# Kernel tuning notes

Measured on AMD Instinct MI355X. Metric: run time of the kernel, lower is better.

## Reference

```python
import jax, jax.numpy as jnp
import numpy as np

N_STATE = 2048
N_HEAD = 16
HEAD_DIM = N_STATE // N_HEAD  # 128
ROPE_THETA = 10000.0


def setup_inputs() -> dict:
    key = jax.random.key(0)
    ks = jax.random.split(key, 8)
    B, S, D = 2, 2048, N_STATE
    scale = 1.0 / np.sqrt(D)
    x = jax.random.normal(ks[0], (B, S, D), dtype=jnp.float32)
    Wq = jax.random.normal(ks[1], (D, D), dtype=jnp.float32) * scale
    bq = jnp.zeros((D,), dtype=jnp.float32)
    Wk = jax.random.normal(ks[2], (D, D), dtype=jnp.float32) * scale  # key has no bias
    Wv = jax.random.normal(ks[3], (D, D), dtype=jnp.float32) * scale
    bv = jnp.zeros((D,), dtype=jnp.float32)
    Wo = jax.random.normal(ks[4], (D, D), dtype=jnp.float32) * scale
    bo = jnp.zeros((D,), dtype=jnp.float32)
    return {"x": x, "Wq": Wq, "bq": bq, "Wk": Wk, "Wv": Wv, "bv": bv, "Wo": Wo, "bo": bo}


def _rope(t, pos):
    # t: [B, S, H, hd]; torchtune-style interleaved rotary (pairs of adjacent dims)
    hd = t.shape[-1]
    inv_freq = 1.0 / (ROPE_THETA ** (jnp.arange(0, hd, 2, dtype=jnp.float32) / hd))  # [hd/2]
    ang = pos[:, None] * inv_freq[None, :]                    # [S, hd/2]
    cos = jnp.cos(ang)[None, :, None, :].astype(t.dtype)       # [1,S,1,hd/2]
    sin = jnp.sin(ang)[None, :, None, :].astype(t.dtype)
    t1 = t[..., 0::2]
    t2 = t[..., 1::2]
    rot = jnp.stack([t1 * cos - t2 * sin, t2 * cos + t1 * sin], axis=-1)
    return rot.reshape(t.shape)


def reference(x, Wq, bq, Wk, Wv, bv, Wo, bo):
    B, S, D = x.shape
    H, hd = N_HEAD, D // N_HEAD
    q = (x @ Wq.T + bq).reshape(B, S, H, hd)
    k = (x @ Wk.T).reshape(B, S, H, hd)
    v = (x @ Wv.T + bv).reshape(B, S, H, hd)
    pos = jnp.arange(S, dtype=jnp.float32)
    q = _rope(q, pos)
    k = _rope(k, pos)
    # [B,H,S,hd]
    q = q.transpose(0, 2, 1, 3)
    k = k.transpose(0, 2, 1, 3)
    v = v.transpose(0, 2, 1, 3)
    scale = 1.0 / jnp.sqrt(jnp.asarray(hd, dtype=x.dtype))
    scores = jnp.einsum('bhqd,bhkd->bhqk', q, k) * scale       # [B,H,S,S]
    causal = jnp.tril(jnp.ones((S, S), dtype=bool))
    scores = jnp.where(causal[None, None], scores, jnp.finfo(scores.dtype).min)
    probs = jax.nn.softmax(scores, axis=-1)
    a = jnp.einsum('bhqk,bhkd->bhqd', probs, v)                # [B,H,S,hd]
    a = a.transpose(0, 2, 1, 3).reshape(B, S, D)
    return a @ Wo.T + bo
```

## Files before the change

### kernel.cpp

```cpp
#include <hip/hip_runtime.h>
#include <stdint.h>

typedef float f32x4 __attribute__((ext_vector_type(4)));
typedef __bf16 bf16x8 __attribute__((ext_vector_type(8)));
typedef unsigned short us8 __attribute__((ext_vector_type(8)));
typedef unsigned short us4 __attribute__((ext_vector_type(4)));
typedef unsigned int u32;

#define MFMA16(A, B, C) __builtin_amdgcn_mfma_f32_16x16x32_bf16( \
    __builtin_bit_cast(bf16x8, (A)), __builtin_bit_cast(bf16x8, (B)), (C), 0, 0, 0)

__device__ __forceinline__ unsigned short f2bf(float f) {
  u32 u = __builtin_bit_cast(u32, f);
  u = u + 0x7fffu + ((u >> 16) & 1u);
  return (unsigned short)(u >> 16);
}
__device__ __forceinline__ float bf2f(unsigned short b) {
  u32 u = ((u32)b) << 16;
  return __builtin_bit_cast(float, u);
}
__device__ __forceinline__ void gload16(const void* g, void* lds) {
  __builtin_amdgcn_global_load_lds((const __attribute__((address_space(1))) u32*)g,
                                   (__attribute__((address_space(3))) u32*)lds, 16, 0, 0);
}

__global__ __launch_bounds__(256) void convert_all(
    const float* __restrict__ x, const float* __restrict__ wq, const float* __restrict__ wk,
    const float* __restrict__ wv, const float* __restrict__ wo,
    unsigned short* __restrict__ xb, unsigned short* __restrict__ wcat,
    unsigned short* __restrict__ wob, float2* __restrict__ tab) {
  if (blockIdx.x >= 2048) {
    int t0 = ((int)blockIdx.x - 2048) * 2048 + (int)threadIdx.x * 8;
#pragma unroll
    for (int j = 0; j < 8; ++j) {
      int idx = t0 + j;
      int s = idx >> 6, i = idx & 63;
      float ang = (float)s * exp2f(-(float)i * 0.2076205059304703f);
      float sv, cv;
      sincosf(ang, &sv, &cv);
      tab[idx] = make_float2(cv, sv);
    }
    return;
  }
  int tid = blockIdx.x * 256 + threadIdx.x;
  int nth = 2048 * 256;
  const float* srcs[5] = {x, wq, wk, wv, wo};
  unsigned short* dsts[5] = {xb, wcat, wcat + 4194304, wcat + 8388608, wob};
  const int n4s[5] = {2097152, 1048576, 1048576, 1048576, 1048576};
#pragma unroll
  for (int sg = 0; sg < 5; ++sg) {
    const float4* s = (const float4*)srcs[sg];
    us4* d = (us4*)dsts[sg];
    int n4 = n4s[sg];
    for (int i = tid; i < n4; i += nth) {
      float4 v = s[i];
      us4 o;
      o[0] = f2bf(v.x); o[1] = f2bf(v.y); o[2] = f2bf(v.z); o[3] = f2bf(v.w);
      d[i] = o;
    }
  }
}

template <int EPI>
__global__ __launch_bounds__(512, 2) void gemmsw(
    const unsigned short* __restrict__ A, const unsigned short* __restrict__ B,
    int nTN, int N,
    float* __restrict__ outF, const float* __restrict__ bias,
    unsigned short* __restrict__ qb, unsigned short* __restrict__ kb,
    unsigned short* __restrict__ vtb, const float* __restrict__ bq,
    const float* __restrict__ bv, const float2* __restrict__ tab) {
  constexpr int KT = 32;
  __shared__ alignas(16) char L[114688];
  char* Lp = L;
  int bid = (int)blockIdx.x, nwg = (int)gridDim.x;
  {
    int qq = nwg >> 3;
    int xcd = bid & 7, idx = bid >> 3;
    bid = xcd * qq + idx;
  }
  int tm = bid / nTN, tn = bid % nTN;
  int t = (int)threadIdx.x, l = t & 63, w = t >> 6;
  int g = l >> 4, ln = l & 15;
  int wr = w >> 2, wc = w & 3;
  int lr = l >> 3, lc = l & 7;
  int scol = lc ^ lr;
  const unsigned short* pAs = A + (size_t)(tm * 256 + w * 8 + lr) * 2048 + scol * 8;
  const unsigned short* pBs = B + (size_t)(tn * 192 + w * 8 + lr) * 2048 + scol * 8;

  f32x4 acc[2][3][4] = {};
  us8 af[2][4][2], bf[2];

#define FENCE asm volatile("" ::: "memory")
#define BAR do { FENCE; __builtin_amdgcn_s_barrier(); FENCE; } while (0)
#define VMW_(n) asm volatile("s_waitcnt vmcnt(" #n ")" ::: "memory")
#define VMW(n) VMW_(n)
#define STA(i, kt, bufsel) do { if ((kt) < KT)                                \
    gload16(pAs + (size_t)(i) * 131072 + (size_t)(kt) * 64,                   \
            Lp + (bufsel) * 57344 + (i) * 8192 + w * 1024); } while (0)
#define STB(i, kt, bufsel) do { if ((kt) < KT)                                \
    gload16(pBs + (size_t)(i) * 131072 + (size_t)(kt) * 64,                   \
            Lp + (bufsel) * 57344 + 32768 + (i) * 8192 + w * 1024); } while (0)
#define RD_AALL(bufsel) do {                                                  \
    _Pragma("unroll") for (int mh = 0; mh < 2; ++mh)                          \
    _Pragma("unroll") for (int mf = 0; mf < 4; ++mf)                          \
    _Pragma("unroll") for (int kc = 0; kc < 2; ++kc)                          \
      af[mh][mf][kc] = *(const us8*)(Lp + (bufsel) * 57344 +                  \
          (wr * 128 + mh * 64 + mf * 16 + ln) * 128 +                         \
          ((kc * 64 + g * 16) ^ ((ln & 7) << 4)));                            \
  } while (0)
#define RD_B(nh_, bufsel) do {                                                \
    _Pragma("unroll") for (int kc = 0; kc < 2; ++kc)                          \
      bf[kc] = *(const us8*)(Lp + (bufsel) * 57344 + 32768 +                  \
          ((nh_) * 64 + wc * 16 + ln) * 128 +                                 \
          ((kc * 64 + g * 16) ^ ((ln & 7) << 4)));                            \
  } while (0)
#define MMF(nh_) do {                                                         \
    __builtin_amdgcn_s_setprio(1);                                            \
    _Pragma("unroll") for (int kc = 0; kc < 2; ++kc)                          \
    _Pragma("unroll") for (int mh = 0; mh < 2; ++mh)                          \
    _Pragma("unroll") for (int mf = 0; mf < 4; ++mf)                          \
      acc[mh][nh_][mf] = MFMA16(af[mh][mf][kc], bf[kc], acc[mh][nh_][mf]);    \
    __builtin_amdgcn_s_setprio(0);                                            \
  } while (0)
#define TILE(kt, b, VM0, VM1, VMB) do {                                       \
   RD_AALL(b); RD_B(0, b);                                             \
          STA(0, (kt) + 1, (b) ^ 1); STA(1, (kt) + 1, (b) ^ 1);               \
          STA(2, (kt) + 1, (b) ^ 1); STA(3, (kt) + 1, (b) ^ 1);               \
          STB(0, (kt) + 1, (b) ^ 1);                                          \
          BAR; MMF(0); VMW(VM0); BAR;                                         \
   RD_B(1, b);                                                         \
          STB(1, (kt) + 1, (b) ^ 1);                                          \
          BAR; MMF(1); VMW(VM1); BAR;                                         \
   RD_B(2, b);                                                         \
          STB(2, (kt) + 1, (b) ^ 1);                                          \
          MMF(2); VMW(VMB); BAR;                                              \
} while (0)

  STA(0, 0, 0); STA(1, 0, 0); STA(2, 0, 0); STA(3, 0, 0); STB(0, 0, 0);
  STB(1, 0, 0); STB(2, 0, 0);
  VMW(2); BAR;

#pragma unroll 1
  for (int kt = 0; kt < 30; kt += 2) {
    TILE(kt, 0, 6, 6, 2);
    TILE(kt + 1, 1, 6, 6, 2);
  }
  TILE(30, 0, 6, 6, 2);
  TILE(31, 1, 1, 0, 0);

#undef TILE
#undef MMF
#undef RD_B
#undef RD_AALL
#undef STB
#undef STA
#undef VMW
#undef VMW_
#undef BAR
#undef FENCE

  if (EPI == 1) {
#pragma unroll
    for (int mh = 0; mh < 2; ++mh)
#pragma unroll
    for (int nh = 0; nh < 3; ++nh)
#pragma unroll
    for (int mf = 0; mf < 4; ++mf) {
      int n = tn * 192 + nh * 64 + wc * 16 + ln;
      float bz = bias[n];
      int m0 = tm * 256 + wr * 128 + mh * 64 + mf * 16 + g * 4;
#pragma unroll
      for (int r = 0; r < 4; ++r)
        outF[(size_t)(m0 + r) * N + n] = acc[mh][nh][mf][r] + bz;
    }
  } else {
#pragma unroll
    for (int mh = 0; mh < 2; ++mh)
#pragma unroll
    for (int nh = 0; nh < 3; ++nh)
#pragma unroll
    for (int mf = 0; mf < 4; ++mf) {
      int n6 = tn * 192 + nh * 64 + wc * 16 + ln;
      int sel = n6 >> 11, d = n6 & 2047, h = d >> 7, hd = d & 127;
      int m0 = tm * 256 + wr * 128 + mh * 64 + mf * 16 + g * 4;
      int b = m0 >> 11, s0 = m0 & 2047;
      if (sel == 2) {
        float badd = bv[d];
        us4 pk;
#pragma unroll
        for (int r = 0; r < 4; ++r) pk[r] = f2bf(acc[mh][nh][mf][r] + badd);
        *(us4*)&vtb[((size_t)(b * 16 + h) * 128 + hd) * 2048 + s0] = pk;
      } else {
        unsigned short* dst = sel ? kb : qb;
        float badd = sel ? 0.f : bq[d];
        int odd = hd & 1;
#pragma unroll
        for (int r = 0; r < 4; ++r) {
          float val = acc[mh][nh][mf][r] + badd;
          float pv = __shfl_xor(val, 1);
          float2 cs = tab[((s0 + r) << 6) | (hd >> 1)];
          float rot = odd ? (val * cs.x + pv * cs.y) : (val * cs.x - pv * cs.y);
          dst[((size_t)(b * 16 + h) * 2048 + (s0 + r)) * 128 + hd] = f2bf(rot);
        }
      }
    }
  }
}

template <int EPI>
__global__ __launch_bounds__(512, 2) void gemm2(
    const unsigned short* __restrict__ A, const unsigned short* __restrict__ B,
    int nTN, int N,
    float* __restrict__ outF, const float* __restrict__ bias) {
  constexpr int K = 2048, KT = 64;
  __shared__ alignas(16) char L[4 * 24576];
  int bid = (int)blockIdx.x, nwg = (int)gridDim.x;
  {
    int qq = nwg >> 3;
    int xcd = bid & 7, idx = bid >> 3;
    bid = xcd * qq + idx;
  }
  int tm = bid / nTN, tn = bid % nTN;
  int t = (int)threadIdx.x, l = t & 63, w = t >> 6;
  int g = l >> 4, ln = l & 15;
  int wr = w >> 2, wc = w & 3;
  const unsigned short* Ab =
      A + (size_t)(tm * 128 + w * 16 + (l >> 2)) * K + (((l & 3) ^ ((l >> 4) & 3))) * 8;
  const unsigned short* Bb =
      B + (size_t)(tn * 256 + w * 16 + (l >> 2)) * K + (((l & 3) ^ ((l >> 4) & 3))) * 8;
  f32x4 acc[4][4] = {};

#define STAGE(tile) do {                                                      \
    char* Lb = L + ((tile) & 3) * 24576 + w * 1024;                           \
    int kc = (tile) * 32;                                                     \
    gload16(Ab + kc, Lb);                                                     \
    gload16(Bb + kc, Lb + 8192);                                              \
    gload16(Bb + (size_t)128 * K + kc, Lb + 16384);                           \
  } while (0)

#define GITER(kt, VM) do {                                                    \
    asm volatile("s_waitcnt vmcnt(" #VM ")" ::: "memory");                    \
    __builtin_amdgcn_s_barrier();                                             \
    __builtin_amdgcn_sched_barrier(0);                                        \
    asm volatile("" ::: "memory");                                            \
    if ((kt) + 3 < KT) STAGE((kt) + 3);                                       \
    const unsigned short* Lc = (const unsigned short*)(L + ((kt) & 3) * 24576); \
    us8 af[4], bfr[4];                                                        \
    _Pragma("unroll") for (int mf = 0; mf < 4; ++mf)                          \
      af[mf] = *(const us8*)&Lc[(wr * 64 + mf * 16 + ln) * 32 +               \
                                ((g ^ ((ln >> 2) & 3)) * 8)];                 \
    _Pragma("unroll") for (int nf = 0; nf < 4; ++nf)                          \
      bfr[nf] = *(const us8*)&Lc[4096 + (wc * 64 + nf * 16 + ln) * 32 +       \
                                 ((g ^ ((ln >> 2) & 3)) * 8)];                \
    __builtin_amdgcn_s_setprio(1);                                            \
    _Pragma("unroll") for (int mf = 0; mf < 4; ++mf)                          \
      _Pragma("unroll") for (int nf = 0; nf < 4; ++nf)                        \
        acc[mf][nf] = MFMA16(af[mf], bfr[nf], acc[mf][nf]);                   \
    __builtin_amdgcn_s_setprio(0);                                            \
  } while (0)

  STAGE(0); STAGE(1); STAGE(2);
#pragma unroll 1
  for (int kt = 0; kt < KT - 2; ++kt) GITER(kt, 6);
  GITER(KT - 2, 3);
  GITER(KT - 1, 0);
#undef STAGE
#undef GITER

#pragma unroll
  for (int mf = 0; mf < 4; ++mf)
#pragma unroll
    for (int nf = 0; nf < 4; ++nf) {
      int n = tn * 256 + wc * 64 + nf * 16 + ln;
      float bz = bias[n];
#pragma unroll
      for (int r = 0; r < 4; ++r) {
        int m = tm * 128 + wr * 64 + mf * 16 + g * 4 + r;
        outF[(size_t)m * N + n] = acc[mf][nf][r] + bz;
      }
    }
}

__global__ __launch_bounds__(512) void attn_k(
    const unsigned short* __restrict__ qg, const unsigned short* __restrict__ kg,
    const unsigned short* __restrict__ vtg, unsigned short* __restrict__ ab) {
  __shared__ alignas(16) unsigned short Kl[2][64 * 128];
  __shared__ alignas(16) unsigned short Vl[2][128 * 64];
  __shared__ alignas(16) unsigned short Pl[8][16 * 72];
  int bh = (int)blockIdx.x & 31;
  int pr = (int)blockIdx.x >> 5;
  int t = (int)threadIdx.x, l = t & 63, w = t >> 6;
  int g = l >> 4, ln = l & 15;
  int b = bh >> 4, h = bh & 15;
  const size_t bq0 = (size_t)bh * 2048 * 128;

  const int qbA = pr * 128, qbB = (15 - pr) * 128;
  const int qrowA = qbA + w * 16 + ln, qrowB = qbB + w * 16 + ln;
  us8 qfA[4], qfB[4];
#pragma unroll
  for (int kf = 0; kf < 4; ++kf) {
    qfA[kf] = *(const us8*)&qg[bq0 + (size_t)qrowA * 128 + kf * 32 + g * 8];
    qfB[kf] = *(const us8*)&qg[bq0 + (size_t)qrowB * 128 + kf * 32 + g * 8];
  }
  f32x4 oA[8] = {}, oB[8] = {};
  float mA = -1e30f, lA = 0.f, mB = -1e30f, lB = 0.f;
  const int nktA = (qbA >> 6) + 2;
  const int nkt  = (qbB >> 6) + 2;

#define STAGEKV(kt1, bsel) do {                                               \
    _Pragma("unroll") for (int i = 0; i < 2; ++i) {                           \
      int fb = i * 8192 + w * 1024;                                           \
      int flat = fb + l * 16;                                                 \
      int row = flat >> 8, colb = flat & 255;                                 \
      int sc = colb ^ ((row & 7) << 4);                                       \
      gload16(kg + (bq0 + (size_t)((kt1) * 64 + row) * 128 + (sc >> 1)),      \
              (char*)Kl + (bsel) * 16384 + fb);                               \
      int rv = flat >> 7, cv2 = flat & 127;                                   \
      int scv = cv2 ^ ((rv & 7) << 4);                                        \
      gload16(vtg + (bq0 + (size_t)rv * 2048 + (kt1) * 64 + (scv >> 1)),      \
              (char*)Vl + (bsel) * 16384 + fb);                               \
    }                                                                         \
  } while (0)

#define COMPUTE(qf, o, mrow, lrow, qrow, kt, bo) do {                         \
    f32x4 st[4];                                                              \
    _Pragma("unroll") for (int kfr = 0; kfr < 4; ++kfr) {                     \
      f32x4 acc = {};                                                         \
      int row = kfr * 16 + ln;                                                \
      int swz = (row & 7) << 4;                                               \
      _Pragma("unroll") for (int kf = 0; kf < 4; ++kf) {                      \
        us8 kfrag = *(const us8*)((const char*)Kl + (bo) + row * 256 +        \
                                  ((kf * 64 + g * 16) ^ swz));                \
        acc = MFMA16(kfrag, qf[kf], acc);                                     \
      }                                                                       \
      st[kfr] = acc;                                                          \
    }                                                                         \
    float pmax = -1e30f;                                                      \
    _Pragma("unroll") for (int kfr = 0; kfr < 4; ++kfr)                       \
    _Pragma("unroll") for (int r = 0; r < 4; ++r) {                           \
      int key = (kt) * 64 + kfr * 16 + g * 4 + r;                             \
      float sv = key <= (qrow) ? st[kfr][r] * 0.08838834764831845f : -1e30f;  \
      st[kfr][r] = sv;                                                        \
      pmax = fmaxf(pmax, sv);                                                 \
    }                                                                         \
    pmax = fmaxf(pmax, __shfl_xor(pmax, 16));                                 \
    pmax = fmaxf(pmax, __shfl_xor(pmax, 32));                                 \
    if (__ballot(pmax > (mrow) + 8.f)) {                                      \
      float mnew = pmax > (mrow) + 8.f ? pmax : (mrow);                       \
      float corr = exp2f(((mrow) - mnew) * 1.44269504f);                      \
      (mrow) = mnew;                                                          \
      (lrow) *= corr;                                                         \
      _Pragma("unroll") for (int r = 0; r < 4; ++r) {                         \
        float cr = __shfl(corr, g * 4 + r);                                   \
        _Pragma("unroll") for (int nf = 0; nf < 8; ++nf) o[nf][r] *= cr;      \
      }                                                                       \
    }                                                                         \
    float lsum = 0.f;                                                         \
    _Pragma("unroll") for (int kfr = 0; kfr < 4; ++kfr) {                     \
      us4 pk;                                                                 \
      _Pragma("unroll") for (int r = 0; r < 4; ++r) {                         \
        float p = exp2f((st[kfr][r] - (mrow)) * 1.44269504f);                 \
        lsum += p;                                                            \
        pk[r] = f2bf(p);                                                      \
      }                                                                       \
      *(us4*)&Pl[w][ln * 72 + kfr * 16 + g * 4] = pk;                         \
    }                                                                         \
    lsum += __shfl_xor(lsum, 16);                                             \
    lsum += __shfl_xor(lsum, 32);                                             \
    (lrow) += lsum;                                                           \
    _Pragma("unroll") for (int kf2 = 0; kf2 < 2; ++kf2) {                     \
      us8 pa = *(const us8*)&Pl[w][ln * 72 + kf2 * 32 + g * 8];               \
      _Pragma("unroll") for (int nf = 0; nf < 8; ++nf) {                      \
        int row = nf * 16 + ln;                                               \
        us8 vb = *(const us8*)((const char*)Vl + (bo) + row * 128 +           \
                               ((kf2 * 64 + g * 16) ^ ((row & 7) << 4)));     \
        o[nf] = MFMA16(pa, vb, o[nf]);                                        \
      }                                                                       \
    }                                                                         \
  } while (0)

  STAGEKV(0, 0);
#pragma unroll 1
  for (int kt = 0; kt < nkt; ++kt) {
    __syncthreads();
    if (kt + 1 < nkt) STAGEKV(kt + 1, (kt + 1) & 1);
    int bo = (kt & 1) * 16384;
    COMPUTE(qfB, oB, mB, lB, qrowB, kt, bo);
    if (kt < nktA) COMPUTE(qfA, oA, mA, lA, qrowA, kt, bo);
  }
#undef COMPUTE
#undef STAGEKV

  {
    float invl = 1.f / lB;
#pragma unroll
    for (int r = 0; r < 4; ++r) {
      float ir = __shfl(invl, g * 4 + r);
      int srow = qbB + w * 16 + g * 4 + r;
      size_t base = ((size_t)b * 2048 + srow) * 2048 + h * 128 + ln;
#pragma unroll
      for (int nf = 0; nf < 8; ++nf) ab[base + (size_t)nf * 16] = f2bf(oB[nf][r] * ir);
    }
  }
  {
    float invl = 1.f / lA;
#pragma unroll
    for (int r = 0; r < 4; ++r) {
      float ir = __shfl(invl, g * 4 + r);
      int srow = qbA + w * 16 + g * 4 + r;
      size_t base = ((size_t)b * 2048 + srow) * 2048 + h * 128 + ln;
#pragma unroll
      for (int nf = 0; nf < 8; ++nf) ab[base + (size_t)nf * 16] = f2bf(oA[nf][r] * ir);
    }
  }
}

extern "C" void kernel_launch(void* const* d_in, const int* in_sizes, int n_in,
                              void* d_out, int out_size, void* d_ws, size_t ws_size,
                              hipStream_t stream) {
  const float* x  = (const float*)d_in[0];
  const float* Wq = (const float*)d_in[1];
  const float* bq = (const float*)d_in[2];
  const float* Wk = (const float*)d_in[3];
  const float* Wv = (const float*)d_in[4];
  const float* bv = (const float*)d_in[5];
  const float* Wo = (const float*)d_in[6];
  const float* bo = (const float*)d_in[7];
  float* out = (float*)d_out;

  unsigned short* ws = (unsigned short*)d_ws;
  unsigned short* xb   = ws;
  unsigned short* wcat = xb + 8388608;
  unsigned short* wob  = wcat + 12582912;
  unsigned short* qb   = wob + 4194304;
  unsigned short* kb   = qb + 8388608;
  unsigned short* vtb  = kb + 8388608;
  float2* tab = (float2*)(vtb + 8388608);

  convert_all<<<2112, 256, 0, stream>>>(x, Wq, Wk, Wv, Wo, xb, wcat, wob, tab);
  gemmsw<0><<<512, 512, 0, stream>>>(xb, wcat, 32, 6144,
                                     nullptr, nullptr, qb, kb, vtb, bq, bv, tab);
  attn_k<<<256, 512, 0, stream>>>(qb, kb, vtb, xb );
  gemm2<1><<<256, 512, 0, stream>>>(xb, wob, 8, 2048, out, bo);
}
```

Before: 252.2 us.

## Split GEMM k-tile into A-half phases to interleave LDS reads with loads

Restructures the per-k-tile schedule of the projection GEMM so A fragments are read one 64-row half at a time and the B fragments for column blocks 0 and 1 are held at once. Global-to-LDS prefetches are regrouped by phase, and the vmcnt wait counts are retuned to match. The aim is to spread LDS reads and async loads more evenly across the three MFMA phases and reduce stalls at barriers. The extra B fragment registers add register pressure, and the changed wait counts must stay consistent with the new load order.

```diff
diff --git a/kernel.cpp b/kernel.cpp
--- a/kernel.cpp
+++ b/kernel.cpp
@@ -88,7 +88,7 @@
   const unsigned short* pBs = B + (size_t)(tn * 192 + w * 8 + lr) * 2048 + scol * 8;
 
   f32x4 acc[2][3][4] = {};
-  us8 af[2][4][2], bf[2];
+  us8 af[2][4][2], bf3[3][2];
 
 #define FENCE asm volatile("" ::: "memory")
 #define BAR do { FENCE; __builtin_amdgcn_s_barrier(); FENCE; } while (0)
@@ -100,58 +100,62 @@
 #define STB(i, kt, bufsel) do { if ((kt) < KT)                                \
     gload16(pBs + (size_t)(i) * 131072 + (size_t)(kt) * 64,                   \
             Lp + (bufsel) * 57344 + 32768 + (i) * 8192 + w * 1024); } while (0)
-#define RD_AALL(bufsel) do {                                                  \
-    _Pragma("unroll") for (int mh = 0; mh < 2; ++mh)                          \
+#define RD_A(mh_, bufsel) do {                                                \
     _Pragma("unroll") for (int mf = 0; mf < 4; ++mf)                          \
     _Pragma("unroll") for (int kc = 0; kc < 2; ++kc)                          \
-      af[mh][mf][kc] = *(const us8*)(Lp + (bufsel) * 57344 +                  \
-          (wr * 128 + mh * 64 + mf * 16 + ln) * 128 +                         \
+      af[mh_][mf][kc] = *(const us8*)(Lp + (bufsel) * 57344 +                 \
+          (wr * 128 + (mh_) * 64 + mf * 16 + ln) * 128 +                      \
           ((kc * 64 + g * 16) ^ ((ln & 7) << 4)));                            \
   } while (0)
 #define RD_B(nh_, bufsel) do {                                                \
     _Pragma("unroll") for (int kc = 0; kc < 2; ++kc)                          \
-      bf[kc] = *(const us8*)(Lp + (bufsel) * 57344 + 32768 +                  \
+      bf3[nh_][kc] = *(const us8*)(Lp + (bufsel) * 57344 + 32768 +            \
           ((nh_) * 64 + wc * 16 + ln) * 128 +                                 \
           ((kc * 64 + g * 16) ^ ((ln & 7) << 4)));                            \
   } while (0)
-#define MMF(nh_) do {                                                         \
-    __builtin_amdgcn_s_setprio(1);                                            \
+#define MM2(mh_, nh_) do {                                                    \
     _Pragma("unroll") for (int kc = 0; kc < 2; ++kc)                          \
-    _Pragma("unroll") for (int mh = 0; mh < 2; ++mh)                          \
     _Pragma("unroll") for (int mf = 0; mf < 4; ++mf)                          \
-      acc[mh][nh_][mf] = MFMA16(af[mh][mf][kc], bf[kc], acc[mh][nh_][mf]);    \
-    __builtin_amdgcn_s_setprio(0);                                            \
+      acc[mh_][nh_][mf] = MFMA16(af[mh_][mf][kc], bf3[nh_][kc],               \
+                                 acc[mh_][nh_][mf]);                          \
   } while (0)
 #define TILE(kt, b, VM0, VM1, VMB) do {                                       \
-   RD_AALL(b); RD_B(0, b);                                             \
-          STA(0, (kt) + 1, (b) ^ 1); STA(1, (kt) + 1, (b) ^ 1);               \
-          STA(2, (kt) + 1, (b) ^ 1); STA(3, (kt) + 1, (b) ^ 1);               \
-          STB(0, (kt) + 1, (b) ^ 1);                                          \
-          BAR; MMF(0); VMW(VM0); BAR;                                         \
-   RD_B(1, b);                                                         \
-          STB(1, (kt) + 1, (b) ^ 1);                                          \
-          BAR; MMF(1); VMW(VM1); BAR;                                         \
+   RD_A(0, b); RD_B(0, b); RD_B(1, b);                                 \
+          STA(0, (kt) + 1, (b) ^ 1); STA(2, (kt) + 1, (b) ^ 1);               \
+          STB(0, (kt) + 1, (b) ^ 1); STB(1, (kt) + 1, (b) ^ 1);               \
+          BAR;                                                                \
+          __builtin_amdgcn_s_setprio(1); MM2(0, 0); MM2(0, 1);                \
+          __builtin_amdgcn_s_setprio(0);                                      \
+          VMW(VM0); BAR;                                                      \
+   RD_A(1, b);                                                         \
+          STA(1, (kt) + 1, (b) ^ 1); STA(3, (kt) + 1, (b) ^ 1);               \
+          BAR;                                                                \
+          __builtin_amdgcn_s_setprio(1); MM2(1, 0); MM2(1, 1);                \
+          __builtin_amdgcn_s_setprio(0);                                      \
+          VMW(VM1); BAR;                                                      \
    RD_B(2, b);                                                         \
           STB(2, (kt) + 1, (b) ^ 1);                                          \
-          MMF(2); VMW(VMB); BAR;                                              \
+          __builtin_amdgcn_s_setprio(1); MM2(0, 2); MM2(1, 2);                \
+          __builtin_amdgcn_s_setprio(0);                                      \
+          VMW(VMB); BAR;                                                      \
 } while (0)
 
-  STA(0, 0, 0); STA(1, 0, 0); STA(2, 0, 0); STA(3, 0, 0); STB(0, 0, 0);
-  STB(1, 0, 0); STB(2, 0, 0);
-  VMW(2); BAR;
+  STA(0, 0, 0); STA(2, 0, 0); STB(0, 0, 0); STB(1, 0, 0);
+  STA(1, 0, 0); STA(3, 0, 0); STB(2, 0, 0);
+  VMW(3); BAR;
 
 #pragma unroll 1
   for (int kt = 0; kt < 30; kt += 2) {
-    TILE(kt, 0, 6, 6, 2);
-    TILE(kt + 1, 1, 6, 6, 2);
-  }
-  TILE(30, 0, 6, 6, 2);
+    TILE(kt, 0, 5, 6, 3);
+    TILE(kt + 1, 1, 5, 6, 3);
+  }
+  TILE(30, 0, 5, 6, 3);
   TILE(31, 1, 1, 0, 0);
 
 #undef TILE
-#undef MMF
+#undef MM2
 #undef RD_B
-#undef RD_AALL
+#undef RD_A
 #undef STB
 #undef STA
 #undef VMW
```

Result: no change. 254.8 us (+1.0%).

## Rewrite output projection GEMM with 64-wide K tiles and 3-buffer interleaved pipeline

Applied to the files above, without the earlier changes.

The output projection GEMM now uses K tiles of 64 instead of 32, cutting the tile count from 64 to 32 and halving the barrier count per K element. It uses three LDS buffers of 48KB with an XOR swizzle over 128-byte rows, and splits the MFMA work into two N phases so the B fragment loads for the second phase overlap the first phase's compute. It uses 144KB of LDS per block while keeping launch_bounds(512,2), which may cap occupancy at one block per CU and limit latency hiding.

```diff
diff --git a/kernel.cpp b/kernel.cpp
--- a/kernel.cpp
+++ b/kernel.cpp
@@ -207,13 +207,13 @@
   }
 }
 
-template <int EPI>
-__global__ __launch_bounds__(512, 2) void gemm2(
+__global__ __launch_bounds__(512, 2) void gemmo(
     const unsigned short* __restrict__ A, const unsigned short* __restrict__ B,
     int nTN, int N,
     float* __restrict__ outF, const float* __restrict__ bias) {
-  constexpr int K = 2048, KT = 64;
-  __shared__ alignas(16) char L[4 * 24576];
+  constexpr int KT = 32;
+  __shared__ alignas(16) char L[147456];
+  char* Lp = L;
   int bid = (int)blockIdx.x, nwg = (int)gridDim.x;
   {
     int qq = nwg >> 3;
@@ -224,61 +224,94 @@
   int t = (int)threadIdx.x, l = t & 63, w = t >> 6;
   int g = l >> 4, ln = l & 15;
   int wr = w >> 2, wc = w & 3;
-  const unsigned short* Ab =
-      A + (size_t)(tm * 128 + w * 16 + (l >> 2)) * K + (((l & 3) ^ ((l >> 4) & 3))) * 8;
-  const unsigned short* Bb =
-      B + (size_t)(tn * 256 + w * 16 + (l >> 2)) * K + (((l & 3) ^ ((l >> 4) & 3))) * 8;
+  int lr = l >> 3, lc = l & 7;
+  int scol = lc ^ lr;
+  const unsigned short* pAs = A + (size_t)(tm * 128 + w * 8 + lr) * 2048 + scol * 8;
+  const unsigned short* pBs = B + (size_t)(tn * 256 + w * 8 + lr) * 2048 + scol * 8;
+
   f32x4 acc[4][4] = {};
-
-#define STAGE(tile) do {                                                      \
-    char* Lb = L + ((tile) & 3) * 24576 + w * 1024;                           \
-    int kc = (tile) * 32;                                                     \
-    gload16(Ab + kc, Lb);                                                     \
-    gload16(Bb + kc, Lb + 8192);                                              \
-    gload16(Bb + (size_t)128 * K + kc, Lb + 16384);                           \
-  } while (0)
-
-#define GITER(kt, VM) do {                                                    \
-    asm volatile("s_waitcnt vmcnt(" #VM ")" ::: "memory");                    \
-    __builtin_amdgcn_s_barrier();                                             \
-    __builtin_amdgcn_sched_barrier(0);                                        \
-    asm volatile("" ::: "memory");                                            \
-    if ((kt) + 3 < KT) STAGE((kt) + 3);                                       \
-    const unsigned short* Lc = (const unsigned short*)(L + ((kt) & 3) * 24576); \
-    us8 af[4], bfr[4];                                                        \
+  us8 af[4][2], bfp[2][2];
+
+#define FENCE asm volatile("" ::: "memory")
+#define BAR do { FENCE; __builtin_amdgcn_s_barrier(); FENCE; } while (0)
+#define VMW_(n) asm volatile("s_waitcnt vmcnt(" #n ")" ::: "memory")
+#define VMW(n) VMW_(n)
+#define OSTA(i, kt, bufsel) do { if ((kt) < KT)                               \
+    gload16(pAs + (size_t)(i) * 131072 + (size_t)(kt) * 64,                   \
+            Lp + (bufsel) * 49152 + (i) * 8192 + w * 1024); } while (0)
+#define OSTB(i, kt, bufsel) do { if ((kt) < KT)                               \
+    gload16(pBs + (size_t)(i) * 131072 + (size_t)(kt) * 64,                   \
+            Lp + (bufsel) * 49152 + 16384 + (i) * 8192 + w * 1024); } while (0)
+#define ORD_A(bufsel) do {                                                    \
     _Pragma("unroll") for (int mf = 0; mf < 4; ++mf)                          \
-      af[mf] = *(const us8*)&Lc[(wr * 64 + mf * 16 + ln) * 32 +               \
-                                ((g ^ ((ln >> 2) & 3)) * 8)];                 \
-    _Pragma("unroll") for (int nf = 0; nf < 4; ++nf)                          \
-      bfr[nf] = *(const us8*)&Lc[4096 + (wc * 64 + nf * 16 + ln) * 32 +       \
-                                 ((g ^ ((ln >> 2) & 3)) * 8)];                \
+    _Pragma("unroll") for (int kc = 0; kc < 2; ++kc)                          \
+      af[mf][kc] = *(const us8*)(Lp + (bufsel) * 49152 +                      \
+          (wr * 64 + mf * 16 + ln) * 128 +                                    \
+          ((kc * 64 + g * 16) ^ ((ln & 7) << 4)));                            \
+  } while (0)
+#define ORD_B2(ph, bufsel) do {                                               \
+    _Pragma("unroll") for (int np = 0; np < 2; ++np)                          \
+    _Pragma("unroll") for (int kc = 0; kc < 2; ++kc)                          \
+      bfp[np][kc] = *(const us8*)(Lp + (bufsel) * 49152 + 16384 +             \
+          (((ph) * 2 + np) * 64 + wc * 16 + ln) * 128 +                       \
+          ((kc * 64 + g * 16) ^ ((ln & 7) << 4)));                            \
+  } while (0)
+#define OMM(ph) do {                                                          \
     __builtin_amdgcn_s_setprio(1);                                            \
+    _Pragma("unroll") for (int np = 0; np < 2; ++np)                          \
+    _Pragma("unroll") for (int kc = 0; kc < 2; ++kc)                          \
     _Pragma("unroll") for (int mf = 0; mf < 4; ++mf)                          \
-      _Pragma("unroll") for (int nf = 0; nf < 4; ++nf)                        \
-        acc[mf][nf] = MFMA16(af[mf], bfr[nf], acc[mf][nf]);                   \
+      acc[(ph) * 2 + np][mf] = MFMA16(af[mf][kc], bfp[np][kc],                \
+                                      acc[(ph) * 2 + np][mf]);                \
     __builtin_amdgcn_s_setprio(0);                                            \
   } while (0)
-
-  STAGE(0); STAGE(1); STAGE(2);
+#define OTILE(kt, bc, bs, VMB) do {                                           \
+   ORD_A(bc); ORD_B2(0, bc);                                           \
+          OSTA(0, (kt) + 2, bs); OSTA(1, (kt) + 2, bs);                       \
+          OSTB(0, (kt) + 2, bs); OSTB(1, (kt) + 2, bs);                       \
+          OSTB(2, (kt) + 2, bs); OSTB(3, (kt) + 2, bs);                       \
+          BAR; OMM(0); BAR;                                                   \
+   ORD_B2(1, bc); OMM(1); VMW(VMB); BAR;                               \
+} while (0)
+
+  OSTA(0, 0, 0); OSTA(1, 0, 0); OSTB(0, 0, 0); OSTB(1, 0, 0);
+  OSTB(2, 0, 0); OSTB(3, 0, 0);
+  OSTA(0, 1, 1); OSTA(1, 1, 1); OSTB(0, 1, 1); OSTB(1, 1, 1);
+  OSTB(2, 1, 1); OSTB(3, 1, 1);
+  VMW(6); BAR;
+
 #pragma unroll 1
-  for (int kt = 0; kt < KT - 2; ++kt) GITER(kt, 6);
-  GITER(KT - 2, 3);
-  GITER(KT - 1, 0);
-#undef STAGE
-#undef GITER
-
-#pragma unroll
-  for (int mf = 0; mf < 4; ++mf)
-#pragma unroll
-    for (int nf = 0; nf < 4; ++nf) {
-      int n = tn * 256 + wc * 64 + nf * 16 + ln;
-      float bz = bias[n];
-#pragma unroll
-      for (int r = 0; r < 4; ++r) {
-        int m = tm * 128 + wr * 64 + mf * 16 + g * 4 + r;
-        outF[(size_t)m * N + n] = acc[mf][nf][r] + bz;
-      }
-    }
+  for (int j = 0; j < 10; ++j) {
+    int k0 = j * 3;
+    OTILE(k0 + 0, 0, 2, 6);
+    OTILE(k0 + 1, 1, 0, 6);
+    OTILE(k0 + 2, 2, 1, 6);
+  }
+  OTILE(30, 0, 2, 0);
+  OTILE(31, 1, 0, 0);
+
+#undef OTILE
+#undef OMM
+#undef ORD_B2
+#undef ORD_A
+#undef OSTB
+#undef OSTA
+#undef VMW
+#undef VMW_
+#undef BAR
+#undef FENCE
+
+#pragma unroll
+  for (int nh = 0; nh < 4; ++nh)
+#pragma unroll
+  for (int mf = 0; mf < 4; ++mf) {
+    int n = tn * 256 + nh * 64 + wc * 16 + ln;
+    float bz = bias[n];
+    int m0 = tm * 128 + wr * 64 + mf * 16 + g * 4;
+#pragma unroll
+    for (int r = 0; r < 4; ++r)
+      outF[(size_t)(m0 + r) * N + n] = acc[nh][mf][r] + bz;
+  }
 }
 
 __global__ __launch_bounds__(512) void attn_k(
@@ -441,5 +474,5 @@
   gemmsw<0><<<512, 512, 0, stream>>>(xb, wcat, 32, 6144,
                                      nullptr, nullptr, qb, kb, vtb, bq, bv, tab);
   attn_k<<<256, 512, 0, stream>>>(qb, kb, vtb, xb );
-  gemm2<1><<<256, 512, 0, stream>>>(xb, wob, 8, 2048, out, bo);
-}
+  gemmo<<<256, 512, 0, stream>>>(xb, wob, 8, 2048, out, bo);
+}
```

Measured after the change: 249.0 us (median of 2 runs). About the same (-1.3%).
